# Performance work log

Hardware: AMD Instinct MI355X
Metric: run time of the kernel (lower is better)

Reference implementation:

```python
import jax, jax.numpy as jnp
import numpy as np

N = 10000        # nodes
E = 320000       # edges (before self-loops)
IN = 128         # in_channels
HID = 128        # hidden_channels per head
HEADS = 4
OUT = 512        # out_channels (final layer, 1 head, no concat)
SLOPE = 0.2      # PyG GATConv negative_slope default


def setup_inputs() -> dict:
    key = jax.random.key(0)
    ks = jax.random.split(key, 16)
    s = 0.05
    inp = {
        "x": jax.random.normal(ks[0], (N, IN), dtype=jnp.float32),
        "edge_index": jax.random.randint(ks[1], (2, E), 0, N, dtype=jnp.int32),
        # layer 1: IN -> HEADS*HID, concat
        "W1": jax.random.normal(ks[2], (IN, HEADS * HID), dtype=jnp.float32) * s,
        "a_src1": jax.random.normal(ks[3], (1, HEADS, HID), dtype=jnp.float32) * s,
        "a_dst1": jax.random.normal(ks[4], (1, HEADS, HID), dtype=jnp.float32) * s,
        "b1": jnp.zeros((HEADS * HID,), dtype=jnp.float32),
        # layer 2: HEADS*HID -> HEADS*HID, concat
        "W2": jax.random.normal(ks[5], (HEADS * HID, HEADS * HID), dtype=jnp.float32) * s,
        "a_src2": jax.random.normal(ks[6], (1, HEADS, HID), dtype=jnp.float32) * s,
        "a_dst2": jax.random.normal(ks[7], (1, HEADS, HID), dtype=jnp.float32) * s,
        "b2": jnp.zeros((HEADS * HID,), dtype=jnp.float32),
        # layer 3: HEADS*HID -> OUT, heads=1, mean (no concat)
        "W3": jax.random.normal(ks[8], (HEADS * HID, OUT), dtype=jnp.float32) * s,
        "a_src3": jax.random.normal(ks[9], (1, 1, OUT), dtype=jnp.float32) * s,
        "a_dst3": jax.random.normal(ks[10], (1, 1, OUT), dtype=jnp.float32) * s,
        "b3": jnp.zeros((OUT,), dtype=jnp.float32),
    }
    return inp


def gat_layer(x, src, dst, W, a_src, a_dst, bias, heads, ch, concat):
    n = x.shape[0]
    h = (x @ W).reshape(n, heads, ch)                 # [N,H,C]
    al_s = jnp.sum(h * a_src, axis=-1)                # [N,H]
    al_d = jnp.sum(h * a_dst, axis=-1)                # [N,H]
    logits = jax.nn.leaky_relu(al_s[src] + al_d[dst], SLOPE)  # [E,H]
    # segment softmax over incoming edges of each destination node
    logits = logits - jax.ops.segment_max(logits, dst, num_segments=n)[dst]
    e = jnp.exp(logits)
    denom = jax.ops.segment_sum(e, dst, num_segments=n)[dst]
    alpha = e / denom                                  # [E,H]
    out = jax.ops.segment_sum(h[src] * alpha[:, :, None], dst, num_segments=n)  # [N,H,C]
    out = out.reshape(n, heads * ch) if concat else out.mean(axis=1)
    return out + bias


def reference(x, edge_index, W1, a_src1, a_dst1, b1, W2, a_src2, a_dst2, b2,
              W3, a_src3, a_dst3, b3):
    n = x.shape[0]
    loop = jnp.arange(n, dtype=edge_index.dtype)       # PyG add_self_loops=True
    src = jnp.concatenate([edge_index[0], loop])
    dst = jnp.concatenate([edge_index[1], loop])
    h = jax.nn.relu(gat_layer(x, src, dst, W1, a_src1, a_dst1, b1, HEADS, HID, True))
    h = jax.nn.relu(gat_layer(h, src, dst, W2, a_src2, a_dst2, b2, HEADS, HID, True))
    return gat_layer(h, src, dst, W3, a_src3, a_dst3, b3, 1, OUT, False)
```

## Files before the change

kernel.cpp:

```cpp
#include <hip/hip_runtime.h>

#define NSLOPE 0.2f
#define CAP 128

typedef __bf16 bf16x8 __attribute__((ext_vector_type(8)));
typedef __bf16 bf16x4 __attribute__((ext_vector_type(4)));
typedef __bf16 bf16x2 __attribute__((ext_vector_type(2)));
typedef float  f32x4  __attribute__((ext_vector_type(4)));
typedef _Float16 half2v __attribute__((ext_vector_type(2)));

static __device__ __forceinline__ float dot2f(unsigned p, unsigned a, float c){
#if __has_builtin(__builtin_amdgcn_fdot2)
  return __builtin_amdgcn_fdot2(__builtin_bit_cast(half2v, p),
                                __builtin_bit_cast(half2v, a), c, false);
#else
  half2v ph = __builtin_bit_cast(half2v, p), ah = __builtin_bit_cast(half2v, a);
  return c + (float)ph[0]*(float)ah[0] + (float)ph[1]*(float)ah[1];
#endif
}


__global__ void fill_kernel(const int* __restrict__ ei, int E,
                            int* cnt, int* __restrict__ col){
  int i = blockIdx.x*blockDim.x + threadIdx.x;
  if (i < E){
    int s = ei[i], d = ei[E + i];
    int slot = atomicAdd(&cnt[d], 1);
    if (slot < CAP) col[(d << 7) + slot] = s;
  }
}

__device__ __forceinline__ void wsplit_body(
    const float* __restrict__ W, __bf16* __restrict__ Bt, int K, int Nc,
    int kb, int nb, float (*hi_s)[33]){
  int tx = threadIdx.x & 31, ty = threadIdx.x >> 5;
  int k0 = kb * 32, n0 = nb * 32;
#pragma unroll
  for (int i = 0; i < 4; i++){
    int r = ty + i*8;
    hi_s[r][tx] = (float)(__bf16)W[(size_t)(k0 + r)*Nc + n0 + tx];
  }
  __syncthreads();
  const size_t Kx16 = (size_t)K * 16;
#pragma unroll
  for (int i = 0; i < 4; i++){
    int n = ty + i*8;
    int r = n0 + n;
    size_t a = (size_t)(r >> 4)*Kx16 + (size_t)(k0 >> 5)*512
             + (size_t)((r & 15) + 16*(tx >> 3))*8 + (tx & 7);
    Bt[a] = (__bf16)hi_s[tx][n];
  }
}

__global__ __launch_bounds__(256) void prep_kernel(
    const float* __restrict__ x, __bf16* __restrict__ X2,
    const float* __restrict__ W1, __bf16* __restrict__ B1t,
    const float* __restrict__ W2, __bf16* __restrict__ B2t,
    const float* __restrict__ W3, __bf16* __restrict__ B3t,
    int* __restrict__ cnt, int* __restrict__ col,
    float* __restrict__ albase, int N){
  __shared__ float hi_s[32][33];
  int b = blockIdx.x, t = threadIdx.x;
  int gid = b*256 + t;
  if (gid < N){
    cnt[gid] = 1;
    col[gid << 7] = gid;
  }
  if (gid*4 < N*18) *(float4*)(albase + gid*4) = make_float4(0.f,0.f,0.f,0.f);

  const int nb_split = (N*32 + 255) / 256;
  if (b < nb_split){
    int i = gid * 4;
    if (i < N*128){
      int n = i >> 7, c = i & 127;
      float4 v = *(const float4*)(x + i);
      float f[4] = {v.x, v.y, v.z, v.w};
      bf16x4 h;
#pragma unroll
      for (int u = 0; u < 4; u++) h[u] = (__bf16)f[u];
      size_t a = (size_t)(n >> 4)*2048 + (size_t)(c >> 5)*512
               + (size_t)((n & 15) + 16*((c >> 3) & 3))*8 + (c & 7);
      *(bf16x4*)(X2 + a) = h;
    }
  } else if (b < nb_split + 64){
    int bb = b - nb_split;
    wsplit_body(W1, B1t, 128, 512, bb & 3, bb >> 2, hi_s);
  } else if (b < nb_split + 64 + 256){
    int bb = b - nb_split - 64;
    wsplit_body(W2, B2t, 512, 512, bb & 15, bb >> 4, hi_s);
  } else {
    int bb = b - nb_split - 320;
    wsplit_body(W3, B3t, 512, 512, bb & 15, bb >> 4, hi_s);
  }
}

template<int H>
__global__ __launch_bounds__(256) void gemm_mfma(
    const __bf16* __restrict__ A2f, const __bf16* __restrict__ B2f,
    _Float16* __restrict__ Hb, const float* __restrict__ asrc,
    const float* __restrict__ adst, float* __restrict__ al_s,
    float* __restrict__ al_d, int M, int K2){
  int t = threadIdx.x, w = t >> 6, lane = t & 63;
  int mm = lane & 15, q = lane >> 4;

  int bid = blockIdx.x;
  int idx = bid >> 3;
  int cb = idx & 3;
  int rowblk = (bid & 7) + ((idx >> 2) << 3);
  if (rowblk * 64 >= M) return;
  int bm = rowblk * 64, bn = cb * 128;
  int wr = w & 1, wc = w >> 1;

  const int nf = K2 >> 5;
  const int rbmax = (M >> 4) - 1;
  const __bf16* pA0; const __bf16* pA1;
  const __bf16* pB0; const __bf16* pB1; const __bf16* pB2; const __bf16* pB3;
  {
    int rb0 = (bm >> 4) + wr*2;     rb0 = (rb0 <= rbmax) ? rb0 : rbmax;
    int rb1 = (bm >> 4) + wr*2 + 1; rb1 = (rb1 <= rbmax) ? rb1 : rbmax;
    pA0 = A2f + (size_t)rb0*nf*512 + lane*8;
    pA1 = A2f + (size_t)rb1*nf*512 + lane*8;
    int rbB = (bn >> 4) + wc*4;
    pB0 = B2f + (size_t)(rbB+0)*nf*512 + lane*8;
    pB1 = B2f + (size_t)(rbB+1)*nf*512 + lane*8;
    pB2 = B2f + (size_t)(rbB+2)*nf*512 + lane*8;
    pB3 = B2f + (size_t)(rbB+3)*nf*512 + lane*8;
  }

  f32x4 acc[2][4];
#pragma unroll
  for (int i = 0; i < 2; i++)
#pragma unroll
    for (int j = 0; j < 4; j++)
#pragma unroll
      for (int r = 0; r < 4; r++) acc[i][j][r] = 0.f;

#pragma unroll 4
  for (int f = 0; f < nf; f++){
    bf16x8 a0 = *(const bf16x8*)(pA0 + (size_t)f*512);
    bf16x8 a1 = *(const bf16x8*)(pA1 + (size_t)f*512);
    bf16x8 b0 = *(const bf16x8*)(pB0 + (size_t)f*512);
    bf16x8 b1 = *(const bf16x8*)(pB1 + (size_t)f*512);
    bf16x8 b2 = *(const bf16x8*)(pB2 + (size_t)f*512);
    bf16x8 b3 = *(const bf16x8*)(pB3 + (size_t)f*512);
    acc[0][0] = __builtin_amdgcn_mfma_f32_16x16x32_bf16(a0, b0, acc[0][0], 0, 0, 0);
    acc[0][1] = __builtin_amdgcn_mfma_f32_16x16x32_bf16(a0, b1, acc[0][1], 0, 0, 0);
    acc[0][2] = __builtin_amdgcn_mfma_f32_16x16x32_bf16(a0, b2, acc[0][2], 0, 0, 0);
    acc[0][3] = __builtin_amdgcn_mfma_f32_16x16x32_bf16(a0, b3, acc[0][3], 0, 0, 0);
    acc[1][0] = __builtin_amdgcn_mfma_f32_16x16x32_bf16(a1, b0, acc[1][0], 0, 0, 0);
    acc[1][1] = __builtin_amdgcn_mfma_f32_16x16x32_bf16(a1, b1, acc[1][1], 0, 0, 0);
    acc[1][2] = __builtin_amdgcn_mfma_f32_16x16x32_bf16(a1, b2, acc[1][2], 0, 0, 0);
    acc[1][3] = __builtin_amdgcn_mfma_f32_16x16x32_bf16(a1, b3, acc[1][3], 0, 0, 0);
  }

  float as_v[4], ad_v[4];
#pragma unroll
  for (int j2 = 0; j2 < 4; j2++){
    int colc = bn + (wc*4 + j2)*16 + mm;
    as_v[j2] = asrc[colc];
    ad_v[j2] = adst[colc];
  }
  const int h = (H == 4) ? (bn >> 7) : 0;
#pragma unroll
  for (int i2 = 0; i2 < 2; i2++){
    int rbase = bm + (wr*2 + i2)*16 + q*4;
#pragma unroll
    for (int j2 = 0; j2 < 4; j2++){
      int colc = bn + (wc*4 + j2)*16 + mm;
#pragma unroll
      for (int r = 0; r < 4; r++){
        int row = rbase + r;
        if (row < M) Hb[(size_t)row*512 + colc] = (_Float16)acc[i2][j2][r];
      }
    }
#pragma unroll
    for (int r = 0; r < 4; r++){
      float ps = acc[i2][0][r]*as_v[0] + acc[i2][1][r]*as_v[1]
               + acc[i2][2][r]*as_v[2] + acc[i2][3][r]*as_v[3];
      float pd = acc[i2][0][r]*ad_v[0] + acc[i2][1][r]*ad_v[1]
               + acc[i2][2][r]*ad_v[2] + acc[i2][3][r]*ad_v[3];
#pragma unroll
      for (int off = 1; off < 16; off <<= 1){
        ps += __shfl_xor(ps, off);
        pd += __shfl_xor(pd, off);
      }
      int row = rbase + r;
      if (mm == 0 && row < M){
        atomicAdd(&al_s[(size_t)row*H + h], ps);
        atomicAdd(&al_d[(size_t)row*H + h], pd);
      }
    }
  }
}

template<int H, int MODE>
__global__ __launch_bounds__(64) void aggregate_slice(
    const _Float16* __restrict__ Hb, const float* __restrict__ al_s,
    const float* __restrict__ al_d, const int* __restrict__ cnt,
    const int* __restrict__ col, const float* __restrict__ bias,
    float* __restrict__ outF, __bf16* __restrict__ fA,
    int nidx, int N){
  __shared__ int      src_s[64];
  __shared__ _Float16 a_sh[64];
  int g = blockIdx.x;
  int x = g & 7, idx = g >> 3;
  int s = x >> 1, half = x & 1;
  int d = half * nidx + idx;
  if (d >= N) return;
  int lane = threadIdx.x;
  const int hh = (H == 1) ? 0 : s;
  const float ald = al_d[(size_t)d*H + hh];
  int deg = cnt[d]; deg = (deg < CAP) ? deg : CAP;
  int start = d << 7;

  int sc0 = 0, sc1 = 0;
  float v0f = -1e30f, v1f = -1e30f;
  if (lane < deg){
    sc0 = col[start + lane];
    float v = al_s[(size_t)sc0*H + hh] + ald;
    v0f = (v > 0.f) ? v : NSLOPE * v;
  }
  if (64 + lane < deg){
    sc1 = col[start + 64 + lane];
    float v = al_s[(size_t)sc1*H + hh] + ald;
    v1f = (v > 0.f) ? v : NSLOPE * v;
  }
  float mx = fmaxf(v0f, v1f);
#pragma unroll
  for (int off = 32; off > 0; off >>= 1)
    mx = fmaxf(mx, __shfl_xor(mx, off));

  float e0 = (lane < deg)      ? __expf(v0f - mx) : 0.f;
  float e1 = (64 + lane < deg) ? __expf(v1f - mx) : 0.f;
  float lsum = e0 + e1;
#pragma unroll
  for (int off = 32; off > 0; off >>= 1)
    lsum += __shfl_xor(lsum, off);

  const unsigned* __restrict__ Hb32 = (const unsigned*)Hb;
  const unsigned coffu = s*64 + lane;
  float accx = 0.f, accy = 0.f;

  int cc0 = (deg < 64) ? deg : 64;
  src_s[lane] = sc0;
  a_sh[lane]  = (_Float16)e0;
  for (int chunk = 0; ; chunk++){
    int cnt2 = (chunk == 0) ? cc0 : (deg - 64);
    int npair = cnt2 >> 1;
    int j = 0;
    for (; j + 2 <= npair; j += 2){
      int s0 = src_s[2*j],     s1 = src_s[2*j+1];
      int s2 = src_s[2*j+2],   s3 = src_s[2*j+3];
      unsigned a01 = *(const unsigned*)&a_sh[2*j];
      unsigned a23 = *(const unsigned*)&a_sh[2*j+2];
      unsigned u0 = Hb32[(size_t)s0*256 + coffu];
      unsigned u1 = Hb32[(size_t)s1*256 + coffu];
      unsigned u2 = Hb32[(size_t)s2*256 + coffu];
      unsigned u3 = Hb32[(size_t)s3*256 + coffu];
      unsigned pc  = (u0 & 0x0000ffffu) | (u1 << 16);
      unsigned pc1 = (u0 >> 16) | (u1 & 0xffff0000u);
      unsigned qc  = (u2 & 0x0000ffffu) | (u3 << 16);
      unsigned qc1 = (u2 >> 16) | (u3 & 0xffff0000u);
      accx = dot2f(pc,  a01, accx);
      accy = dot2f(pc1, a01, accy);
      accx = dot2f(qc,  a23, accx);
      accy = dot2f(qc1, a23, accy);
    }
    for (; j < npair; j++){
      int s0 = src_s[2*j], s1 = src_s[2*j+1];
      unsigned a01 = *(const unsigned*)&a_sh[2*j];
      unsigned u0 = Hb32[(size_t)s0*256 + coffu];
      unsigned u1 = Hb32[(size_t)s1*256 + coffu];
      unsigned pc  = (u0 & 0x0000ffffu) | (u1 << 16);
      unsigned pc1 = (u0 >> 16) | (u1 & 0xffff0000u);
      accx = dot2f(pc,  a01, accx);
      accy = dot2f(pc1, a01, accy);
    }
    if (cnt2 & 1){
      int sl = src_s[cnt2 - 1];
      float al = (float)a_sh[cnt2 - 1];
      unsigned ul = Hb32[(size_t)sl*256 + coffu];
      half2v hv = __builtin_bit_cast(half2v, ul);
      accx += al * (float)hv[0];
      accy += al * (float)hv[1];
    }
    if (chunk == 1 || deg <= 64) break;
    src_s[lane] = sc1;
    a_sh[lane]  = (_Float16)e1;
  }

  float invd = 1.f / lsum;
  int c = s*128 + lane*2;
  float2 bv = *(const float2*)(bias + c);
  float r0 = accx * invd + bv.x;
  float r1 = accy * invd + bv.y;
  if (MODE == 1){
    r0 = fmaxf(r0, 0.f); r1 = fmaxf(r1, 0.f);
    bf16x2 hv; hv[0] = (__bf16)r0; hv[1] = (__bf16)r1;
    size_t a = (size_t)(d >> 4)*8192 + (size_t)(c >> 5)*512
             + (size_t)((d & 15) + 16*((c >> 3) & 3))*8 + (c & 7);
    *(bf16x2*)(fA + a) = hv;
  } else {
    *(float2*)(outF + (size_t)d*512 + c) = make_float2(r0, r1);
  }
}

extern "C" void kernel_launch(void* const* d_in, const int* in_sizes, int n_in,
                              void* d_out, int out_size, void* d_ws, size_t ws_size,
                              hipStream_t stream){
  const float* x   = (const float*)d_in[0];
  const int*   ei  = (const int*)  d_in[1];
  const float* W1  = (const float*)d_in[2];
  const float* as1 = (const float*)d_in[3];
  const float* ad1 = (const float*)d_in[4];
  const float* b1  = (const float*)d_in[5];
  const float* W2  = (const float*)d_in[6];
  const float* as2 = (const float*)d_in[7];
  const float* ad2 = (const float*)d_in[8];
  const float* b2  = (const float*)d_in[9];
  const float* W3  = (const float*)d_in[10];
  const float* as3 = (const float*)d_in[11];
  const float* ad3 = (const float*)d_in[12];
  const float* b3  = (const float*)d_in[13];
  float* out = (float*)d_out;

  const int N = in_sizes[0] / 128;
  const int E = in_sizes[1] / 2;
  const int nidx = (N + 1) / 2;

  __bf16* feat2  = (__bf16*)d_ws;
  __bf16* X2     = feat2 + (size_t)N*512;
  float*  albase = (float*)(X2 + (size_t)N*128);
  float*  als1   = albase;
  float*  ald1   = als1 + (size_t)N*4;
  float*  als2   = ald1 + (size_t)N*4;
  float*  ald2   = als2 + (size_t)N*4;
  float*  als3   = ald2 + (size_t)N*4;
  float*  ald3   = als3 + (size_t)N;
  int*    cnt    = (int*)(ald3 + (size_t)N);
  int*    col    = cnt + N;
  uintptr_t p  = (uintptr_t)(col + (size_t)N*CAP);
  p = (p + 15) & ~(uintptr_t)15;
  __bf16* B1t = (__bf16*)p;
  __bf16* B2t = B1t + 512*128;
  __bf16* B3t = B2t + 512*512;
  _Float16* Hb = (_Float16*)(B3t + 512*512);

  const int nb_split = (N*32 + 255)/256;
  const int pgrid = nb_split + 64 + 256 + 256;

  prep_kernel<<<pgrid, 256, 0, stream>>>(x, X2, W1, B1t, W2, B2t, W3, B3t,
                                         cnt, col, albase, N);
  fill_kernel<<<(E+255)/256, 256, 0, stream>>>(ei, E, cnt, col);

  const int nrb = (N + 63)/64;
  const int ggrid = (((nrb + 7) >> 3) << 3) * 4;
  const int agrid = nidx * 8;

  gemm_mfma<4><<<ggrid, 256, 0, stream>>>(X2, B1t, Hb, as1, ad1, als1, ald1, N, 128);
  aggregate_slice<4,1><<<agrid, 64, 0, stream>>>(Hb, als1, ald1, cnt, col, b1,
      (float*)nullptr, feat2, nidx, N);

  gemm_mfma<4><<<ggrid, 256, 0, stream>>>(feat2, B2t, Hb, as2, ad2, als2, ald2, N, 512);
  aggregate_slice<4,1><<<agrid, 64, 0, stream>>>(Hb, als2, ald2, cnt, col, b2,
      (float*)nullptr, feat2, nidx, N);

  gemm_mfma<1><<<ggrid, 256, 0, stream>>>(feat2, B3t, Hb, as3, ad3, als3, ald3, N, 512);
  aggregate_slice<1,0><<<agrid, 64, 0, stream>>>(Hb, als3, ald3, cnt, col, b3,
      out, (__bf16*)nullptr, nidx, N);
}
```

Measured before the change: 266.9 us.

## Precompute normalized attention weights in a separate alpha kernel per layer

Adds an alpha_kernel that computes the segment softmax once per destination node for all heads and stores normalized fp16 weights. Previously the aggregation computed it redundantly in every channel-slice block. The aggregate kernel now just loads these weights, which cuts repeated gathers of al_s, the exp calls and the reductions. In exchange it adds three kernel launches and an extra global write and read of the alpha buffer. Normalizing before the fp16 conversion also changes rounding slightly.

Result: slower. 279.0 us (+4.5%).

```diff
diff --git a/kernel.cpp b/kernel.cpp
--- a/kernel.cpp
+++ b/kernel.cpp
@@ -193,13 +193,78 @@
   }
 }
 
+template<int H>
+__global__ __launch_bounds__(256) void alpha_kernel(
+    const float* __restrict__ al_s, const float* __restrict__ al_d,
+    const int* __restrict__ cnt, const int* __restrict__ col,
+    _Float16* __restrict__ alpha, int N){
+  int t = threadIdx.x, w = t >> 6, lane = t & 63;
+  int d = blockIdx.x*4 + w;
+  if (d >= N) return;
+  int deg = cnt[d]; deg = (deg < CAP) ? deg : CAP;
+  int start = d << 7;
+
+  float adv[H], l0[H], l1[H];
+#pragma unroll
+  for (int h = 0; h < H; h++){
+    adv[h] = al_d[(size_t)d*H + h];
+    l0[h] = -1e30f; l1[h] = -1e30f;
+  }
+  if (lane < deg){
+    int sc = col[start + lane];
+    if (H == 4){
+      float4 v4 = *(const float4*)(al_s + (size_t)sc*4);
+      float vv[4] = {v4.x, v4.y, v4.z, v4.w};
+#pragma unroll
+      for (int h = 0; h < H; h++){
+        float v = vv[h] + adv[h];
+        l0[h] = (v > 0.f) ? v : NSLOPE*v;
+      }
+    } else {
+      float v = al_s[sc] + adv[0];
+      l0[0] = (v > 0.f) ? v : NSLOPE*v;
+    }
+  }
+  if (64 + lane < deg){
+    int sc = col[start + 64 + lane];
+    if (H == 4){
+      float4 v4 = *(const float4*)(al_s + (size_t)sc*4);
+      float vv[4] = {v4.x, v4.y, v4.z, v4.w};
+#pragma unroll
+      for (int h = 0; h < H; h++){
+        float v = vv[h] + adv[h];
+        l1[h] = (v > 0.f) ? v : NSLOPE*v;
+      }
+    } else {
+      float v = al_s[sc] + adv[0];
+      l1[0] = (v > 0.f) ? v : NSLOPE*v;
+    }
+  }
+#pragma unroll
+  for (int h = 0; h < H; h++){
+    float mx = fmaxf(l0[h], l1[h]);
+#pragma unroll
+    for (int off = 32; off > 0; off >>= 1)
+      mx = fmaxf(mx, __shfl_xor(mx, off));
+    float e0 = (lane < deg)      ? __expf(l0[h] - mx) : 0.f;
+    float e1 = (64 + lane < deg) ? __expf(l1[h] - mx) : 0.f;
+    float ss = e0 + e1;
+#pragma unroll
+    for (int off = 32; off > 0; off >>= 1)
+      ss += __shfl_xor(ss, off);
+    float inv = 1.f / ss;
+    _Float16* op = alpha + ((size_t)d*H + h)*128;
+    if (lane < deg)      op[lane]      = (_Float16)(e0*inv);
+    if (64 + lane < deg) op[64 + lane] = (_Float16)(e1*inv);
+  }
+}
+
 template<int H, int MODE>
 __global__ __launch_bounds__(64) void aggregate_slice(
-    const _Float16* __restrict__ Hb, const float* __restrict__ al_s,
-    const float* __restrict__ al_d, const int* __restrict__ cnt,
-    const int* __restrict__ col, const float* __restrict__ bias,
-    float* __restrict__ outF, __bf16* __restrict__ fA,
-    int nidx, int N){
+    const _Float16* __restrict__ Hb, const _Float16* __restrict__ alpha,
+    const int* __restrict__ cnt, const int* __restrict__ col,
+    const float* __restrict__ bias, float* __restrict__ outF,
+    __bf16* __restrict__ fA, int nidx, int N){
   __shared__ int      src_s[64];
   __shared__ _Float16 a_sh[64];
   int g = blockIdx.x;
@@ -209,33 +274,14 @@
   if (d >= N) return;
   int lane = threadIdx.x;
   const int hh = (H == 1) ? 0 : s;
-  const float ald = al_d[(size_t)d*H + hh];
   int deg = cnt[d]; deg = (deg < CAP) ? deg : CAP;
   int start = d << 7;
+  const _Float16* __restrict__ ap = alpha + ((size_t)d*H + hh)*128;
 
   int sc0 = 0, sc1 = 0;
-  float v0f = -1e30f, v1f = -1e30f;
-  if (lane < deg){
-    sc0 = col[start + lane];
-    float v = al_s[(size_t)sc0*H + hh] + ald;
-    v0f = (v > 0.f) ? v : NSLOPE * v;
-  }
-  if (64 + lane < deg){
-    sc1 = col[start + 64 + lane];
-    float v = al_s[(size_t)sc1*H + hh] + ald;
-    v1f = (v > 0.f) ? v : NSLOPE * v;
-  }
-  float mx = fmaxf(v0f, v1f);
-#pragma unroll
-  for (int off = 32; off > 0; off >>= 1)
-    mx = fmaxf(mx, __shfl_xor(mx, off));
-
-  float e0 = (lane < deg)      ? __expf(v0f - mx) : 0.f;
-  float e1 = (64 + lane < deg) ? __expf(v1f - mx) : 0.f;
-  float lsum = e0 + e1;
-#pragma unroll
-  for (int off = 32; off > 0; off >>= 1)
-    lsum += __shfl_xor(lsum, off);
+  _Float16 a0 = (_Float16)0.f, a1 = (_Float16)0.f;
+  if (lane < deg){ sc0 = col[start + lane]; a0 = ap[lane]; }
+  if (64 + lane < deg){ sc1 = col[start + 64 + lane]; a1 = ap[64 + lane]; }
 
   const unsigned* __restrict__ Hb32 = (const unsigned*)Hb;
   const unsigned coffu = s*64 + lane;
@@ -243,7 +289,7 @@
 
   int cc0 = (deg < 64) ? deg : 64;
   src_s[lane] = sc0;
-  a_sh[lane]  = (_Float16)e0;
+  a_sh[lane]  = a0;
   for (int chunk = 0; ; chunk++){
     int cnt2 = (chunk == 0) ? cc0 : (deg - 64);
     int npair = cnt2 >> 1;
@@ -286,14 +332,13 @@
     }
     if (chunk == 1 || deg <= 64) break;
     src_s[lane] = sc1;
-    a_sh[lane]  = (_Float16)e1;
-  }
-
-  float invd = 1.f / lsum;
+    a_sh[lane]  = a1;
+  }
+
   int c = s*128 + lane*2;
   float2 bv = *(const float2*)(bias + c);
-  float r0 = accx * invd + bv.x;
-  float r1 = accy * invd + bv.y;
+  float r0 = accx + bv.x;
+  float r1 = accy + bv.y;
   if (MODE == 1){
     r0 = fmaxf(r0, 0.f); r1 = fmaxf(r1, 0.f);
     bf16x2 hv; hv[0] = (__bf16)r0; hv[1] = (__bf16)r1;
@@ -345,6 +390,7 @@
   __bf16* B2t = B1t + 512*128;
   __bf16* B3t = B2t + 512*512;
   _Float16* Hb = (_Float16*)(B3t + 512*512);
+  _Float16* alphaA = Hb + (size_t)N*512;
 
   const int nb_split = (N*32 + 255)/256;
   const int pgrid = nb_split + 64 + 256 + 256;
@@ -356,16 +402,20 @@
   const int nrb = (N + 63)/64;
   const int ggrid = (((nrb + 7) >> 3) << 3) * 4;
   const int agrid = nidx * 8;
+  const int algrid = (N + 3)/4;
 
   gemm_mfma<4><<<ggrid, 256, 0, stream>>>(X2, B1t, Hb, as1, ad1, als1, ald1, N, 128);
-  aggregate_slice<4,1><<<agrid, 64, 0, stream>>>(Hb, als1, ald1, cnt, col, b1,
+  alpha_kernel<4><<<algrid, 256, 0, stream>>>(als1, ald1, cnt, col, alphaA, N);
+  aggregate_slice<4,1><<<agrid, 64, 0, stream>>>(Hb, alphaA, cnt, col, b1,
       (float*)nullptr, feat2, nidx, N);
 
   gemm_mfma<4><<<ggrid, 256, 0, stream>>>(feat2, B2t, Hb, as2, ad2, als2, ald2, N, 512);
-  aggregate_slice<4,1><<<agrid, 64, 0, stream>>>(Hb, als2, ald2, cnt, col, b2,
+  alpha_kernel<4><<<algrid, 256, 0, stream>>>(als2, ald2, cnt, col, alphaA, N);
+  aggregate_slice<4,1><<<agrid, 64, 0, stream>>>(Hb, alphaA, cnt, col, b2,
       (float*)nullptr, feat2, nidx, N);
 
   gemm_mfma<1><<<ggrid, 256, 0, stream>>>(feat2, B3t, Hb, as3, ad3, als3, ald3, N, 512);
-  aggregate_slice<1,0><<<agrid, 64, 0, stream>>>(Hb, als3, ald3, cnt, col, b3,
+  alpha_kernel<1><<<algrid, 256, 0, stream>>>(als3, ald3, cnt, col, alphaA, N);
+  aggregate_slice<1,0><<<agrid, 64, 0, stream>>>(Hb, alphaA, cnt, col, b3,
       out, (__bf16*)nullptr, nidx, N);
 }
```
